# Kernel tuning notes

Hardware: AMD Instinct MI355X
Metric: run time of the kernel (lower is better)

Reference implementation:

```python
import jax, jax.numpy as jnp
import numpy as np

GROUPS = 16
EPS = 1e-5


def _dcn_v2(x, offset, mask, weight):
    """Modulated deformable 3x3 conv, stride=1, pad=1, no bias.
    x: [B,C,H,W], offset: [B,18,H,W] (dy,dx interleaved per kernel point),
    mask: [B,9,H,W] (modulation scalars), weight: [O,C,3,3]."""
    B, C, H, W = x.shape
    O = weight.shape[0]
    K = 9
    # kernel-point displacements, row-major (kh, kw): k = kh*3 + kw
    ky = jnp.repeat(jnp.arange(3) - 1, 3).astype(x.dtype)   # [9]
    kx = jnp.tile(jnp.arange(3) - 1, 3).astype(x.dtype)      # [9]
    dy = offset[:, 0::2]  # [B,9,H,W]
    dx = offset[:, 1::2]  # [B,9,H,W]
    hh = jnp.arange(H, dtype=x.dtype)
    ww = jnp.arange(W, dtype=x.dtype)
    # sampling coordinates (stride=1, pad=1)
    ys = hh[None, None, :, None] + ky[None, :, None, None] + dy  # [B,9,H,W]
    xs = ww[None, None, None, :] + kx[None, :, None, None] + dx  # [B,9,H,W]

    y0 = jnp.floor(ys)
    x0 = jnp.floor(xs)
    wy1 = ys - y0
    wx1 = xs - x0
    y0i = y0.astype(jnp.int32)
    x0i = x0.astype(jnp.int32)

    flat = x.reshape(B, C, H * W)

    def gather(yi, xi, w):
        # yi, xi, w: [B,9,H,W]; zero-padding outside the image
        valid = (yi >= 0) & (yi < H) & (xi >= 0) & (xi < W)
        idx = jnp.clip(yi, 0, H - 1) * W + jnp.clip(xi, 0, W - 1)  # [B,9,H,W]
        g = jnp.take_along_axis(flat, idx.reshape(B, 1, K * H * W), axis=2)
        g = g.reshape(B, C, K, H, W)
        return g * (w * valid.astype(x.dtype))[:, None]  # [B,C,9,H,W]

    val = (gather(y0i,     x0i,     (1 - wy1) * (1 - wx1))
         + gather(y0i,     x0i + 1, (1 - wy1) * wx1)
         + gather(y0i + 1, x0i,     wy1 * (1 - wx1))
         + gather(y0i + 1, x0i + 1, wy1 * wx1))
    val = val * mask[:, None]  # modulation
    # implicit GEMM: [B,C,9,H,W] x [O,C,9] -> [B,O,H,W]
    return jnp.einsum('bckhw,ock->bohw', val, weight.reshape(O, C, K))


def _group_norm(x, gamma, beta):
    B, C, H, W = x.shape
    xg = x.reshape(B, GROUPS, C // GROUPS, H, W)
    mu = xg.mean(axis=(2, 3, 4), keepdims=True)
    var = xg.var(axis=(2, 3, 4), keepdims=True)
    xn = ((xg - mu) * jax.lax.rsqrt(var + EPS)).reshape(B, C, H, W)
    return xn * gamma[None, :, None, None] + beta[None, :, None, None]


def setup_inputs() -> dict:
    key = jax.random.key(0)
    k1, k2, k3, k4 = jax.random.split(key, 4)
    B, C, O, H, W = 8, 256, 256, 64, 64
    x = jax.random.normal(k1, (B, C, H, W), dtype=jnp.float32)
    offset = jax.random.normal(k2, (B, 18, H, W), dtype=jnp.float32)
    mask = jax.random.uniform(k3, (B, 9, H, W), dtype=jnp.float32)
    weight = jax.random.normal(k4, (O, C, 3, 3), dtype=jnp.float32) * (1.0 / np.sqrt(C * 9))
    gamma = jnp.ones((O,), dtype=jnp.float32)
    beta = jnp.zeros((O,), dtype=jnp.float32)
    return {"x": x, "offset": offset, "mask": mask, "weight": weight,
            "gamma": gamma, "beta": beta}


def reference(x, offset, mask, weight, gamma, beta):
    out = _dcn_v2(x, offset, mask, weight)
    return _group_norm(out, gamma, beta)
```

## Files before the change

kernel.cpp:

```cpp
#include <hip/hip_runtime.h>
#include <stdint.h>


#define B_ 8
#define C_ 256
#define O_ 256
#define H_ 64
#define W_ 64
#define HW_ 4096
#define KTOT 2304
#define GROUPS_ 16
#define EPS_ 1e-5f
#define NSTEP 36
#define VROW 72

typedef float  f32x4  __attribute__((ext_vector_type(4)));
typedef short  short8 __attribute__((ext_vector_type(8)));
typedef unsigned int   u32;
typedef unsigned short u16;

#define XT_BYTES   (B_*HW_*C_*2)
#define WIMG_OFF   XT_BYTES
#define WIMG_BYTES (72*16*64*16)
#define STATS_OFF  (WIMG_OFF + WIMG_BYTES)

__device__ __forceinline__ u32 bf16r(float f) {
    u32 u = __float_as_uint(f);
    return (u + 0x7fffu + ((u >> 16) & 1u)) >> 16;
}
__device__ __forceinline__ u32 pack_bf16x2(float lo, float hi) {
    return bf16r(lo) | (bf16r(hi) << 16);
}
__device__ __forceinline__ u32 pack_perm(float lo, float hi) {
    return __builtin_amdgcn_perm(__float_as_uint(hi), __float_as_uint(lo), 0x07060302u);
}
__device__ __forceinline__ float bflo(u32 u) { return __uint_as_float(u << 16); }
__device__ __forceinline__ float bfhi_f(u32 u) { return __uint_as_float(u); }

__device__ __forceinline__ void barrier_lds() {
    asm volatile("s_waitcnt lgkmcnt(0)\n\ts_barrier" ::: "memory");
}

__global__ void k_prep(const float* __restrict__ x, u16* __restrict__ xt,
                       const float* __restrict__ w, u16* __restrict__ wimg,
                       float* __restrict__ stats) {
    const int bid = blockIdx.x;
    const int tid = threadIdx.x;
    if (bid >= 2048 + 288) {
        stats[tid] = 0.f;
        return;
    }
    if (bid < 2048) {
        __shared__ float tile[64][65];
        const int b = bid >> 8, ct = (bid >> 6) & 3, pt = bid & 63;
#pragma unroll
        for (int pass = 0; pass < 4; ++pass) {
            const int r  = (tid >> 4) + pass * 16;
            const int pq = tid & 15;
            const f32x4 v = *(const f32x4*)&x[(((size_t)(b * C_ + ct * 64 + r)) << 12)
                                              + pt * 64 + pq * 4];
            tile[r][pq * 4 + 0] = v.x;
            tile[r][pq * 4 + 1] = v.y;
            tile[r][pq * 4 + 2] = v.z;
            tile[r][pq * 4 + 3] = v.w;
        }
        __syncthreads();
        const int pr = tid >> 2, cg = tid & 3;
        u32 o[8];
#pragma unroll
        for (int j = 0; j < 8; ++j)
            o[j] = pack_bf16x2(tile[cg * 16 + 2 * j][pr], tile[cg * 16 + 2 * j + 1][pr]);
        u16* dst = &xt[(((size_t)b << 12) + pt * 64 + pr) * 256 + ct * 64 + cg * 16];
        *(uint4*)dst       = *(uint4*)&o[0];
        *(uint4*)(dst + 8) = *(uint4*)&o[4];
    } else {
        const int item = (bid - 2048) * 256 + tid;
        if (item < 72 * 1024) {
            const int sub = item >> 10;
            const int idx = item & 1023;
            const int k  = sub >> 3;
            const int c0 = (sub & 7) * 32;
            const int lane = idx & 63;
            const int frag = idx >> 6;
            const int col = lane & 15, quad = lane >> 4;
            const int n = frag * 16 + col;
            const float* src = w + (size_t)n * KTOT + (size_t)(c0 + quad * 8) * 9 + k;
            u32 o[4];
#pragma unroll
            for (int j = 0; j < 4; ++j)
                o[j] = pack_bf16x2(src[(size_t)(2 * j) * 9], src[(size_t)(2 * j + 1) * 9]);
            *(uint4*)&wimg[((size_t)sub * 1024 + idx) * 8] = *(uint4*)o;
        }
    }
}

__device__ __forceinline__ void issue_gather(const u16* __restrict__ cb,
                                             const float* __restrict__ mwp,
                                             const int* __restrict__ mip,
                                             int gpos, uint4 g[4], f32x4& mw) {
    mw = *(const f32x4*)&mwp[gpos * 4];
    const int4 ix = *(const int4*)&mip[gpos * 4];
    g[0] = *(const uint4*)(cb + ix.x);
    g[1] = *(const uint4*)(cb + ix.y);
    g[2] = *(const uint4*)(cb + ix.z);
    g[3] = *(const uint4*)(cb + ix.w);
}

__device__ __forceinline__ void interp_store(const uint4 g[4], f32x4 mw, u16* dst) {
    float s[8];
#pragma unroll
    for (int i = 0; i < 8; ++i) s[i] = 0.f;
    const float ww[4] = {mw.x, mw.y, mw.z, mw.w};
#pragma unroll
    for (int cr = 0; cr < 4; ++cr) {
        const float wg = ww[cr];
        const uint4 a = g[cr];
        s[0] += wg * bflo(a.x);  s[1] += wg * bfhi_f(a.x);
        s[2] += wg * bflo(a.y);  s[3] += wg * bfhi_f(a.y);
        s[4] += wg * bflo(a.z);  s[5] += wg * bfhi_f(a.z);
        s[6] += wg * bflo(a.w);  s[7] += wg * bfhi_f(a.w);
    }
    uint4 pk;
    pk.x = pack_perm(s[0], s[1]);
    pk.y = pack_perm(s[2], s[3]);
    pk.z = pack_perm(s[4], s[5]);
    pk.w = pack_perm(s[6], s[7]);
    *(uint4*)dst = pk;
}

__device__ __forceinline__ void load_wfrags(const u16* __restrict__ wimg, int s,
                                            int wid, int lane, short8 bf[4]) {
#pragma unroll
    for (int kc = 0; kc < 2; ++kc)
#pragma unroll
        for (int ni = 0; ni < 2; ++ni)
            bf[kc * 2 + ni] = *(const short8*)
                &wimg[(((size_t)(2 * s + kc) * 16 + wid * 2 + ni) * 64 + lane) * 8];
}

__launch_bounds__(512, 4)
__global__ void k_dcn(const u16* __restrict__ xt, const u16* __restrict__ wimg,
                      const float* __restrict__ offp, const float* __restrict__ mskp,
                      float* __restrict__ out, float* __restrict__ stats) {
    __shared__ __align__(16) float meta_w[9 * 64 * 4];
    __shared__ __align__(16) int   meta_i[9 * 64 * 4];
    __shared__ __align__(16) u16   lds_v[2][64 * VROW];

    const int tid = threadIdx.x;
    const int gid = blockIdx.x;
    const int b   = gid & 7;
    const int m0  = (gid >> 3) * 64;
    const int lane = tid & 63, wid = tid >> 6;
    const int col = lane & 15, quad = lane >> 4;
    const int gpos = tid >> 3, slot = tid & 7;

    const u16* xtb = xt + ((size_t)b << 20);

    for (int it = tid; it < 576; it += 512) {
        const int pos = it & 63, k = it >> 6;
        const int pg = m0 + pos;
        const int hh = pg >> 6, wwi = pg & 63;
        const float dy = offp[((size_t)(b * 18 + 2 * k) << 12) + pg];
        const float dx = offp[((size_t)(b * 18 + 2 * k + 1) << 12) + pg];
        const float mv = mskp[((size_t)(b * 9 + k) << 12) + pg];
        const float ys = (float)(hh + (k / 3) - 1) + dy;
        const float xs = (float)(wwi + (k % 3) - 1) + dx;
        const float y0f = floorf(ys), x0f = floorf(xs);
        const int y0 = (int)y0f, x0 = (int)x0f;
        const float wy1 = ys - y0f, wx1 = xs - x0f;
        const float wy0 = 1.f - wy1, wx0 = 1.f - wx1;
        const int y1 = y0 + 1, x1 = x0 + 1;
        const float vy0 = (y0 >= 0 && y0 < H_) ? 1.f : 0.f;
        const float vy1 = (y1 >= 0 && y1 < H_) ? 1.f : 0.f;
        const float vx0 = (x0 >= 0 && x0 < W_) ? 1.f : 0.f;
        const float vx1 = (x1 >= 0 && x1 < W_) ? 1.f : 0.f;
        const int y0c = min(max(y0, 0), H_ - 1), y1c = min(max(y1, 0), H_ - 1);
        const int x0c = min(max(x0, 0), W_ - 1), x1c = min(max(x1, 0), W_ - 1);
        meta_w[it * 4 + 0] = mv * wy0 * wx0 * vy0 * vx0;
        meta_w[it * 4 + 1] = mv * wy0 * wx1 * vy0 * vx1;
        meta_w[it * 4 + 2] = mv * wy1 * wx0 * vy1 * vx0;
        meta_w[it * 4 + 3] = mv * wy1 * wx1 * vy1 * vx1;
        meta_i[it * 4 + 0] = (y0c * W_ + x0c) << 8;
        meta_i[it * 4 + 1] = (y0c * W_ + x1c) << 8;
        meta_i[it * 4 + 2] = (y1c * W_ + x0c) << 8;
        meta_i[it * 4 + 3] = (y1c * W_ + x1c) << 8;
    }
    __syncthreads();

    uint4 g2[2][4]; f32x4 mw2[2]; short8 bf[4];
    issue_gather(xtb + 0 + slot * 8, &meta_w[0], &meta_i[0], gpos, g2[0], mw2[0]);
    interp_store(g2[0], mw2[0], &lds_v[0][gpos * VROW + slot * 8]);
    issue_gather(xtb + 64 + slot * 8, &meta_w[0], &meta_i[0], gpos, g2[1], mw2[1]);
    __syncthreads();

    f32x4 acc[4][2];
#pragma unroll
    for (int i = 0; i < 4; ++i)
#pragma unroll
        for (int j = 0; j < 2; ++j) acc[i][j] = (f32x4){0.f, 0.f, 0.f, 0.f};

#pragma unroll 2
    for (int s = 0; s < NSTEP; ++s) {
        const int p = s & 1;

        load_wfrags(wimg, s, wid, lane, bf);

        if (s + 2 < NSTEP) {
            const int sn = s + 2;
            const int kn = sn >> 2, c0n = (sn & 3) * 64;
            issue_gather(xtb + c0n + slot * 8, &meta_w[kn * 256], &meta_i[kn * 256],
                         gpos, g2[p], mw2[p]);
        }

#pragma unroll
        for (int kc = 0; kc < 2; ++kc) {
            short8 af[4];
#pragma unroll
            for (int mi = 0; mi < 4; ++mi)
                af[mi] = *(const short8*)
                    &lds_v[p][(mi * 16 + col) * VROW + kc * 32 + quad * 8];
#pragma unroll
            for (int mi = 0; mi < 4; ++mi)
#pragma unroll
                for (int ni = 0; ni < 2; ++ni)
                    acc[mi][ni] = __builtin_amdgcn_mfma_f32_16x16x32_bf16(
                        af[mi], bf[kc * 2 + ni], acc[mi][ni], 0, 0, 0);
        }

        if (s + 1 < NSTEP)
            interp_store(g2[1 - p], mw2[1 - p], &lds_v[1 - p][gpos * VROW + slot * 8]);

        barrier_lds();
    }

#pragma unroll
    for (int mi = 0; mi < 4; ++mi)
#pragma unroll
        for (int ni = 0; ni < 2; ++ni) {
            const int o  = wid * 32 + ni * 16 + col;
            const int pg = m0 + mi * 16 + quad * 4;
            *(f32x4*)(out + (((size_t)b * O_ + o) << 12) + pg) = acc[mi][ni];
        }

#pragma unroll
    for (int ni = 0; ni < 2; ++ni) {
        float s = 0.f, s2 = 0.f;
#pragma unroll
        for (int mi = 0; mi < 4; ++mi) {
            f32x4 v = acc[mi][ni];
            s  += v.x + v.y + v.z + v.w;
            s2 += v.x * v.x + v.y * v.y + v.z * v.z + v.w * v.w;
        }
#pragma unroll
        for (int d = 32; d > 0; d >>= 1) {
            s  += __shfl_xor(s, d, 64);
            s2 += __shfl_xor(s2, d, 64);
        }
        if (lane == 0) {
            const int gI = wid * 2 + ni;
            atomicAdd(&stats[b * GROUPS_ + gI], s);
            atomicAdd(&stats[128 + b * GROUPS_ + gI], s2);
        }
    }
}

__global__ void k_gn(float* __restrict__ out, const float* __restrict__ stats,
                     const float* __restrict__ gamma, const float* __restrict__ beta) {
    const int blk = blockIdx.x;
    const int b = blk >> 8, o = blk & 255;
    const int gI = b * GROUPS_ + (o >> 4);
    const float n = 65536.f;
    const float mean = stats[gI] / n;
    const float var  = stats[128 + gI] / n - mean * mean;
    const float inv  = rsqrtf(fmaxf(var, 0.f) + EPS_);
    const float scale = inv * gamma[o];
    const float shift = beta[o] - mean * scale;
    f32x4* p = (f32x4*)(out + ((size_t)blk << 12));
    const int t = threadIdx.x;
#pragma unroll
    for (int i = 0; i < 4; ++i) {
        f32x4 v = p[t + i * 256];
        p[t + i * 256] = v * scale + shift;
    }
}

extern "C" void kernel_launch(void* const* d_in, const int* in_sizes, int n_in,
                              void* d_out, int out_size, void* d_ws, size_t ws_size,
                              hipStream_t stream) {
    const float* x     = (const float*)d_in[0];
    const float* offp  = (const float*)d_in[1];
    const float* mskp  = (const float*)d_in[2];
    const float* w     = (const float*)d_in[3];
    const float* gamma = (const float*)d_in[4];
    const float* beta  = (const float*)d_in[5];
    float* outp = (float*)d_out;

    u16*   xt    = (u16*)d_ws;
    u16*   wimg  = (u16*)((char*)d_ws + WIMG_OFF);
    float* stats = (float*)((char*)d_ws + STATS_OFF);

    k_prep<<<dim3(2048 + 288 + 1), dim3(256), 0, stream>>>(x, xt, w, wimg, stats);
    k_dcn<<<dim3(512), dim3(512), 0, stream>>>(xt, wimg, offp, mskp, outp, stats);
    k_gn<<<dim3(2048), dim3(256), 0, stream>>>(outp, stats, gamma, beta);
}
```

Before: 181.2 us.

## Fuse GroupNorm into DCN kernel using a grid-wide atomic barrier

Removes the separate GroupNorm kernel. After each DCN block has added its partial statistics, the block waits on a global atomic counter until all 512 blocks have arrived. It then applies the normalization to the accumulators still held in registers and writes the output once. This avoids a second full read and write of the output plus one kernel launch. It relies on all 512 blocks being resident at the same time (launch bounds of 4 blocks per CU); if they are not, the spin barrier deadlocks.

```diff
diff --git a/kernel.cpp b/kernel.cpp
--- a/kernel.cpp
+++ b/kernel.cpp
@@ -13,6 +13,7 @@
 #define EPS_ 1e-5f
 #define NSTEP 36
 #define VROW 72
+#define NBLK 512
 
 typedef float  f32x4  __attribute__((ext_vector_type(4)));
 typedef short  short8 __attribute__((ext_vector_type(8)));
@@ -43,11 +44,12 @@
 
 __global__ void k_prep(const float* __restrict__ x, u16* __restrict__ xt,
                        const float* __restrict__ w, u16* __restrict__ wimg,
-                       float* __restrict__ stats) {
+                       float* __restrict__ stats, int* __restrict__ cnt) {
     const int bid = blockIdx.x;
     const int tid = threadIdx.x;
     if (bid >= 2048 + 288) {
         stats[tid] = 0.f;
+        if (tid == 0) *cnt = 0;
         return;
     }
     if (bid < 2048) {
@@ -141,10 +143,13 @@
 __launch_bounds__(512, 4)
 __global__ void k_dcn(const u16* __restrict__ xt, const u16* __restrict__ wimg,
                       const float* __restrict__ offp, const float* __restrict__ mskp,
-                      float* __restrict__ out, float* __restrict__ stats) {
+                      const float* __restrict__ gamma, const float* __restrict__ beta,
+                      float* __restrict__ out, float* __restrict__ stats,
+                      int* __restrict__ cnt) {
     __shared__ __align__(16) float meta_w[9 * 64 * 4];
     __shared__ __align__(16) int   meta_i[9 * 64 * 4];
     __shared__ __align__(16) u16   lds_v[2][64 * VROW];
+    __shared__ float lds_stats[32];
 
     const int tid = threadIdx.x;
     const int gid = blockIdx.x;
@@ -234,53 +239,56 @@
     }
 
 #pragma unroll
-    for (int mi = 0; mi < 4; ++mi)
-#pragma unroll
-        for (int ni = 0; ni < 2; ++ni) {
-            const int o  = wid * 32 + ni * 16 + col;
-            const int pg = m0 + mi * 16 + quad * 4;
-            *(f32x4*)(out + (((size_t)b * O_ + o) << 12) + pg) = acc[mi][ni];
-        }
-
-#pragma unroll
     for (int ni = 0; ni < 2; ++ni) {
-        float s = 0.f, s2 = 0.f;
+        float s1 = 0.f, s2 = 0.f;
 #pragma unroll
         for (int mi = 0; mi < 4; ++mi) {
             f32x4 v = acc[mi][ni];
-            s  += v.x + v.y + v.z + v.w;
+            s1 += v.x + v.y + v.z + v.w;
             s2 += v.x * v.x + v.y * v.y + v.z * v.z + v.w * v.w;
         }
 #pragma unroll
         for (int d = 32; d > 0; d >>= 1) {
-            s  += __shfl_xor(s, d, 64);
+            s1 += __shfl_xor(s1, d, 64);
             s2 += __shfl_xor(s2, d, 64);
         }
         if (lane == 0) {
             const int gI = wid * 2 + ni;
-            atomicAdd(&stats[b * GROUPS_ + gI], s);
+            atomicAdd(&stats[b * GROUPS_ + gI], s1);
             atomicAdd(&stats[128 + b * GROUPS_ + gI], s2);
         }
     }
-}
-
-__global__ void k_gn(float* __restrict__ out, const float* __restrict__ stats,
-                     const float* __restrict__ gamma, const float* __restrict__ beta) {
-    const int blk = blockIdx.x;
-    const int b = blk >> 8, o = blk & 255;
-    const int gI = b * GROUPS_ + (o >> 4);
-    const float n = 65536.f;
-    const float mean = stats[gI] / n;
-    const float var  = stats[128 + gI] / n - mean * mean;
-    const float inv  = rsqrtf(fmaxf(var, 0.f) + EPS_);
-    const float scale = inv * gamma[o];
-    const float shift = beta[o] - mean * scale;
-    f32x4* p = (f32x4*)(out + ((size_t)blk << 12));
-    const int t = threadIdx.x;
-#pragma unroll
-    for (int i = 0; i < 4; ++i) {
-        f32x4 v = p[t + i * 256];
-        p[t + i * 256] = v * scale + shift;
+
+    __threadfence();
+    __syncthreads();
+    if (tid == 0) {
+        atomicAdd(cnt, 1);
+        while (atomicAdd(cnt, 0) < NBLK) __builtin_amdgcn_s_sleep(8);
+    }
+    __syncthreads();
+
+    if (tid < 32) {
+        const int g = tid & 15, which = tid >> 4;
+        lds_stats[tid] = atomicAdd(&stats[which * 128 + b * GROUPS_ + g], 0.f);
+    }
+    __syncthreads();
+
+#pragma unroll
+    for (int ni = 0; ni < 2; ++ni) {
+        const int o  = wid * 32 + ni * 16 + col;
+        const int gI = wid * 2 + ni;
+        const float mean  = lds_stats[gI] * (1.f / 65536.f);
+        const float var   = lds_stats[16 + gI] * (1.f / 65536.f) - mean * mean;
+        const float inv   = rsqrtf(fmaxf(var, 0.f) + EPS_);
+        const float scale = inv * gamma[o];
+        const float shift = beta[o] - mean * scale;
+#pragma unroll
+        for (int mi = 0; mi < 4; ++mi) {
+            const int pg = m0 + mi * 16 + quad * 4;
+            f32x4 v = acc[mi][ni];
+            v = v * scale + shift;
+            *(f32x4*)(out + (((size_t)b * O_ + o) << 12) + pg) = v;
+        }
     }
 }
 
@@ -298,8 +306,9 @@
     u16*   xt    = (u16*)d_ws;
     u16*   wimg  = (u16*)((char*)d_ws + WIMG_OFF);
     float* stats = (float*)((char*)d_ws + STATS_OFF);
-
-    k_prep<<<dim3(2048 + 288 + 1), dim3(256), 0, stream>>>(x, xt, w, wimg, stats);
-    k_dcn<<<dim3(512), dim3(512), 0, stream>>>(xt, wimg, offp, mskp, outp, stats);
-    k_gn<<<dim3(2048), dim3(256), 0, stream>>>(outp, stats, gamma, beta);
-}
+    int*   cnt   = (int*)((char*)d_ws + STATS_OFF + 1024);
+
+    k_prep<<<dim3(2048 + 288 + 1), dim3(256), 0, stream>>>(x, xt, w, wimg, stats, cnt);
+    k_dcn<<<dim3(NBLK), dim3(512), 0, stream>>>(xt, wimg, offp, mskp, gamma, beta,
+                                                outp, stats, cnt);
+}
```

Result: slower. 233.8 us (+29.0%).
